# Kernel tuning notes

Measured on AMD Instinct MI355X. Metric: run time of the kernel, lower is better.

The kernel has to match this reference:

```python
import jax, jax.numpy as jnp
import numpy as np

H = 512  # hidden_size

def setup_inputs() -> dict:
    key = jax.random.key(0)
    ks = jax.random.split(key, 5)
    B, S = 2, 512
    feats = jax.random.normal(ks[0], (B, S, H), dtype=jnp.float32)
    # torch Linear init ~ U(-1/sqrt(in), 1/sqrt(in)); scaled normals are fine for a reference
    W1 = jax.random.normal(ks[1], (2 * H, H), dtype=jnp.float32) / np.sqrt(2 * H)
    b1 = jnp.zeros((H,), dtype=jnp.float32)
    W2 = jax.random.normal(ks[2], (H, H // 2), dtype=jnp.float32) / np.sqrt(H)
    b2 = jnp.zeros((H // 2,), dtype=jnp.float32)
    W3 = jax.random.normal(ks[3], (H // 2, 1), dtype=jnp.float32) / np.sqrt(H // 2)
    b3 = jnp.zeros((1,), dtype=jnp.float32)
    return {"features": feats, "W1": W1, "b1": b1, "W2": W2, "b2": b2, "W3": W3, "b3": b3}


def reference(features, W1, b1, W2, b2, W3, b3):
    # cat([f_i, f_j]) @ W1 == f_i @ W1[:H] + f_j @ W1[H:]
    # Precompute the two halves once per residue instead of per pair.
    a = jnp.einsum('bsh,hk->bsk', features, W1[:H])          # [B,S,H]
    c = jnp.einsum('bsh,hk->bsk', features, W1[H:])          # [B,S,H]
    h1 = jax.nn.relu(a[:, :, None, :] + c[:, None, :, :] + b1)  # [B,S,S,H]
    # Dropout(0.1) is identity at inference.
    h2 = jax.nn.relu(jnp.einsum('bijh,hk->bijk', h1, W2) + b2)  # [B,S,S,H//2]
    logits = jnp.einsum('bijk,ko->bijo', h2, W3) + b3            # [B,S,S,1]
    return jax.nn.sigmoid(logits[..., 0])                        # [B,S,S]
```

## Files before the change

kernel.cpp:

```cpp
#include <hip/hip_runtime.h>

#define S_DIM 512
#define H_DIM 512
#define NH 256
#define TI 16
#define TJ 8
#define SROW 520

#define AS1 __attribute__((address_space(1)))
#define AS3 __attribute__((address_space(3)))

typedef _Float16 half8 __attribute__((ext_vector_type(8)));
typedef _Float16 half4 __attribute__((ext_vector_type(4)));
typedef float f32x4 __attribute__((ext_vector_type(4)));
typedef float f32x16 __attribute__((ext_vector_type(16)));

__global__ __launch_bounds__(256) void convert_all_kernel(const float* __restrict__ feats,
        const float* __restrict__ W1, const float* __restrict__ W2,
        _Float16* __restrict__ f16, _Float16* __restrict__ w1L, _Float16* __restrict__ w2L) {
    int blk = blockIdx.x;
    if (blk < 512) {
        int t = blk * 256 + threadIdx.x;
        float4 v = ((const float4*)feats)[t];
        half4 h;
        h.x = (_Float16)v.x; h.y = (_Float16)v.y; h.z = (_Float16)v.z; h.w = (_Float16)v.w;
        ((half4*)f16)[t] = h;
    } else if (blk < 768) {
        int t = (blk - 512) * 256 + threadIdx.x;
        int gcb = t >> 10, n = t & 1023;
        const float* src = (n < H_DIM) ? &W1[(size_t)(gcb * 8) * H_DIM + n]
                                       : &W1[(size_t)(H_DIM + gcb * 8) * H_DIM + (n - H_DIM)];
        half8 v;
#pragma unroll
        for (int j = 0; j < 8; j++) v[j] = (_Float16)src[(size_t)j * H_DIM];
        *(half8*)&w1L[((size_t)gcb * 1024 + n) * 8] = v;
    } else {
        int t = (blk - 768) * 256 + threadIdx.x;
        int gcb = t >> 8, n = t & 255;
        half8 v;
#pragma unroll
        for (int j = 0; j < 8; j++) v[j] = (_Float16)W2[(size_t)(gcb * 8 + j) * NH + n];
        *(half8*)&w2L[((size_t)gcb * 256 + n) * 8] = v;
    }
}

__global__ __launch_bounds__(256) void prep_mfma_kernel(const _Float16* __restrict__ f16,
        const _Float16* __restrict__ w1L, const float* __restrict__ b1,
        _Float16* __restrict__ aH, _Float16* __restrict__ cH) {
    const int tid = threadIdx.x, wave = tid >> 6, lane = tid & 63;
    const int m32 = lane & 31, ch = lane >> 5;
    const int m0 = blockIdx.y * 32;
    const int n0w = blockIdx.x * 128 + wave * 32;
    const int n = n0w + m32;

    const _Float16* ap = &f16[(size_t)(m0 + m32) * H_DIM + ch * 8];
    const _Float16* bp = &w1L[((size_t)ch * 1024 + n) * 8];

    f32x16 acc = (f32x16)0.f;
#pragma unroll
    for (int ks = 0; ks < 32; ks++) {
        half8 af = *(const half8*)&ap[ks * 16];
        half8 bf = *(const half8*)&bp[(size_t)ks * 16384];
        acc = __builtin_amdgcn_mfma_f32_32x32x16_f16(af, bf, acc, 0, 0, 0);
    }
    const bool first_half = (n0w < H_DIM);
    const float bias = first_half ? b1[n & (H_DIM - 1)] : 0.f;
#pragma unroll
    for (int r = 0; r < 16; r++) {
        int m = m0 + (r & 3) + 8 * (r >> 2) + 4 * ch;
        float v = acc[r] + bias;
        if (first_half) aH[(size_t)m * H_DIM + n] = (_Float16)v;
        else            cH[(size_t)m * H_DIM + (n - H_DIM)] = (_Float16)v;
    }
}

__global__ __launch_bounds__(512, 4) void pair_kernel(
        const _Float16* __restrict__ aH, const _Float16* __restrict__ cH,
        const _Float16* __restrict__ w2L,
        const float* __restrict__ b2, const float* __restrict__ W3,
        const float* __restrict__ b3, float* __restrict__ out) {
    const int jt = blockIdx.x, it = blockIdx.y, b = blockIdx.z;
    const int i0 = it * TI, j0 = jt * TJ;

    __shared__ __align__(16) _Float16 sa[TI * SROW];
    __shared__ __align__(16) _Float16 sc[TJ * SROW];
    __shared__ float spart[2 * 64 * 32];

    const int tid = threadIdx.x;
    const int wave = tid >> 6, lane = tid & 63;
    const int mg = wave >> 2, ng = wave & 3;
    const int nb = ng * 64;
    const int m32 = lane & 31, ch = lane >> 5;

#pragma unroll
    for (int rr0 = 0; rr0 < 3; rr0++) {
        int rr = rr0 * 8 + wave;
        if (rr < TI) {
            __builtin_amdgcn_global_load_lds(
                (const AS1 unsigned int*)&aH[((size_t)(b * S_DIM + i0 + rr)) * H_DIM + lane * 8],
                (AS3 unsigned int*)&sa[rr * SROW], 16, 0, 0);
        } else {
            int cr = rr - TI;
            __builtin_amdgcn_global_load_lds(
                (const AS1 unsigned int*)&cH[((size_t)(b * S_DIM + j0 + cr)) * H_DIM + lane * 8],
                (AS3 unsigned int*)&sc[cr * SROW], 16, 0, 0);
        }
    }

    const int il0 = mg * 8 + (m32 >> 3);
    const int il1 = il0 + 4;
    const int jl = m32 & 7;
    const _Float16* vaB0 = &sa[il0 * SROW + ch * 8];
    const _Float16* vaB1 = &sa[il1 * SROW + ch * 8];
    const _Float16* vcB  = &sc[jl * SROW + ch * 8];

    f32x16 acc[2][2];
#pragma unroll
    for (int mt = 0; mt < 2; mt++)
#pragma unroll
        for (int nt = 0; nt < 2; nt++) acc[mt][nt] = (f32x16)0.f;

    const _Float16* bp = &w2L[((size_t)ch * 256 + nb + m32) * 8];
    half8 buf0[2], buf1[2];
    buf0[0] = *(const half8*)&bp[0];
    buf0[1] = *(const half8*)&bp[256];
    buf1[0] = *(const half8*)&bp[4096];
    buf1[1] = *(const half8*)&bp[4096 + 256];

    __syncthreads();

#pragma unroll
    for (int ks = 0; ks < 32; ks++) {
        half8 bf0 = (ks & 1) ? buf1[0] : buf0[0];
        half8 bf1 = (ks & 1) ? buf1[1] : buf0[1];
        if (ks < 30) {
            const _Float16* bn = bp + (size_t)(ks + 2) * 4096;
            if (ks & 1) { buf1[0] = *(const half8*)&bn[0]; buf1[1] = *(const half8*)&bn[256]; }
            else        { buf0[0] = *(const half8*)&bn[0]; buf0[1] = *(const half8*)&bn[256]; }
        }
        half8 vc  = *(const half8*)&vcB[ks * 16];
        half8 va0 = *(const half8*)&vaB0[ks * 16];
        half8 va1 = *(const half8*)&vaB1[ks * 16];
        half8 af0 = __builtin_elementwise_max(va0 + vc, (half8)(_Float16)0.f);
        half8 af1 = __builtin_elementwise_max(va1 + vc, (half8)(_Float16)0.f);
        acc[0][0] = __builtin_amdgcn_mfma_f32_32x32x16_f16(af0, bf0, acc[0][0], 0, 0, 0);
        acc[0][1] = __builtin_amdgcn_mfma_f32_32x32x16_f16(af0, bf1, acc[0][1], 0, 0, 0);
        acc[1][0] = __builtin_amdgcn_mfma_f32_32x32x16_f16(af1, bf0, acc[1][0], 0, 0, 0);
        acc[1][1] = __builtin_amdgcn_mfma_f32_32x32x16_f16(af1, bf1, acc[1][1], 0, 0, 0);
    }

    float b2v[2], w3v[2];
#pragma unroll
    for (int nt = 0; nt < 2; nt++) {
        int n = nb + nt * 32 + m32;
        b2v[nt] = b2[n];
        w3v[nt] = W3[n];
    }
#pragma unroll
    for (int mt = 0; mt < 2; mt++)
#pragma unroll
        for (int r = 0; r < 16; r++) {
            float s = 0.f;
#pragma unroll
            for (int nt = 0; nt < 2; nt++) {
                float v = acc[mt][nt][r] + b2v[nt];
                v = v > 0.f ? v : 0.f;
                s += v * w3v[nt];
            }
            s += __shfl_xor(s, 8);
            s += __shfl_xor(s, 16);
            if (m32 < 8) {
                int row = mt * 32 + (r & 3) + 8 * (r >> 2) + 4 * ch;
                int col = ng * 8 + m32;
                spart[mg * 2048 + row * 32 + ((col + row) & 31)] = s;
            }
        }
    __syncthreads();
    {
        const int R = tid >> 2, sub = tid & 3;
        const int mgf = R >> 6, rowf = R & 63;
        const float* base = &spart[mgf * 2048 + rowf * 32];
        float s = 0.f;
#pragma unroll
        for (int k = 0; k < 8; k++) s += base[(sub * 8 + k + rowf) & 31];
        s += __shfl_xor(s, 1);
        s += __shfl_xor(s, 2);
        if (sub == 0) {
            float tot = s + b3[0];
            float sg = 1.f / (1.f + __expf(-tot));
            int i = i0 + (R >> 3), j = j0 + (R & 7);
            out[(size_t)b * S_DIM * S_DIM + (size_t)i * S_DIM + j] = sg;
        }
    }
}

extern "C" void kernel_launch(void* const* d_in, const int* in_sizes, int n_in,
                              void* d_out, int out_size, void* d_ws, size_t ws_size,
                              hipStream_t stream) {
    const float* feats = (const float*)d_in[0];
    const float* W1 = (const float*)d_in[1];
    const float* b1 = (const float*)d_in[2];
    const float* W2 = (const float*)d_in[3];
    const float* b2 = (const float*)d_in[4];
    const float* W3 = (const float*)d_in[5];
    const float* b3 = (const float*)d_in[6];
    float* out = (float*)d_out;

    const int B = in_sizes[0] / (S_DIM * H_DIM);

    char* ws = (char*)d_ws;
    _Float16* f16  = (_Float16*)ws;
    _Float16* aH   = (_Float16*)(ws + (1 << 20));
    _Float16* cH   = (_Float16*)(ws + (2 << 20));
    _Float16* w1L  = (_Float16*)(ws + (3 << 20));
    _Float16* w2L  = (_Float16*)(ws + (4 << 20));

    convert_all_kernel<<<832, 256, 0, stream>>>(feats, W1, W2, f16, w1L, w2L);
    prep_mfma_kernel<<<dim3(8, 32), 256, 0, stream>>>(f16, w1L, b1, aH, cH);
    pair_kernel<<<dim3(S_DIM / TJ, S_DIM / TI, B), 512, 0, stream>>>(aH, cH, w2L, b2, W3, b3, out);
}
```

Measured before the change: 225.9 us.

## Fuse fp32-to-fp16 conversion into prep GEMM and prefetch LDS operands in pair kernel

Removes the separate conversion pass for features and W1: the prep MFMA kernel now reads fp32 directly and converts in registers, with smaller 128-thread blocks on a wider grid. Only W2 is still pre-converted, by a smaller kernel. In the pair kernel, the LDS reads for the a/c rows are software-pipelined one k-step ahead, and the W2 fragments use an indexed double buffer. This trades an extra launch and global round-trip for strided fp32 column reads of W1 in the prep kernel, plus more registers in the pair kernel.

```diff
diff --git a/kernel.cpp b/kernel.cpp
--- a/kernel.cpp
+++ b/kernel.cpp
@@ -11,66 +11,51 @@
 #define AS3 __attribute__((address_space(3)))
 
 typedef _Float16 half8 __attribute__((ext_vector_type(8)));
-typedef _Float16 half4 __attribute__((ext_vector_type(4)));
-typedef float f32x4 __attribute__((ext_vector_type(4)));
 typedef float f32x16 __attribute__((ext_vector_type(16)));
 
-__global__ __launch_bounds__(256) void convert_all_kernel(const float* __restrict__ feats,
-        const float* __restrict__ W1, const float* __restrict__ W2,
-        _Float16* __restrict__ f16, _Float16* __restrict__ w1L, _Float16* __restrict__ w2L) {
-    int blk = blockIdx.x;
-    if (blk < 512) {
-        int t = blk * 256 + threadIdx.x;
-        float4 v = ((const float4*)feats)[t];
-        half4 h;
-        h.x = (_Float16)v.x; h.y = (_Float16)v.y; h.z = (_Float16)v.z; h.w = (_Float16)v.w;
-        ((half4*)f16)[t] = h;
-    } else if (blk < 768) {
-        int t = (blk - 512) * 256 + threadIdx.x;
-        int gcb = t >> 10, n = t & 1023;
-        const float* src = (n < H_DIM) ? &W1[(size_t)(gcb * 8) * H_DIM + n]
-                                       : &W1[(size_t)(H_DIM + gcb * 8) * H_DIM + (n - H_DIM)];
-        half8 v;
-#pragma unroll
-        for (int j = 0; j < 8; j++) v[j] = (_Float16)src[(size_t)j * H_DIM];
-        *(half8*)&w1L[((size_t)gcb * 1024 + n) * 8] = v;
-    } else {
-        int t = (blk - 768) * 256 + threadIdx.x;
-        int gcb = t >> 8, n = t & 255;
-        half8 v;
-#pragma unroll
-        for (int j = 0; j < 8; j++) v[j] = (_Float16)W2[(size_t)(gcb * 8 + j) * NH + n];
-        *(half8*)&w2L[((size_t)gcb * 256 + n) * 8] = v;
-    }
-}
-
-__global__ __launch_bounds__(256) void prep_mfma_kernel(const _Float16* __restrict__ f16,
-        const _Float16* __restrict__ w1L, const float* __restrict__ b1,
+__global__ __launch_bounds__(256) void convert_w2_kernel(const float* __restrict__ W2,
+                                                         _Float16* __restrict__ w2L) {
+    int t = blockIdx.x * 256 + threadIdx.x;
+    int gcb = t >> 8, n = t & 255;
+    half8 v;
+#pragma unroll
+    for (int j = 0; j < 8; j++) v[j] = (_Float16)W2[(size_t)(gcb * 8 + j) * NH + n];
+    *(half8*)&w2L[((size_t)gcb * 256 + n) * 8] = v;
+}
+
+__global__ __launch_bounds__(128) void prep_mfma_kernel(const float* __restrict__ feats,
+        const float* __restrict__ W1, const float* __restrict__ b1,
         _Float16* __restrict__ aH, _Float16* __restrict__ cH) {
     const int tid = threadIdx.x, wave = tid >> 6, lane = tid & 63;
     const int m32 = lane & 31, ch = lane >> 5;
     const int m0 = blockIdx.y * 32;
-    const int n0w = blockIdx.x * 128 + wave * 32;
-    const int n = n0w + m32;
-
-    const _Float16* ap = &f16[(size_t)(m0 + m32) * H_DIM + ch * 8];
-    const _Float16* bp = &w1L[((size_t)ch * 1024 + n) * 8];
+    const int n = blockIdx.x * 64 + wave * 32 + m32;
+    const bool fh = (n < H_DIM);
+    const float* wcol = fh ? &W1[n] : &W1[(size_t)H_DIM * H_DIM + (n - H_DIM)];
+    const float* arow = &feats[(size_t)(m0 + m32) * H_DIM + ch * 8];
 
     f32x16 acc = (f32x16)0.f;
 #pragma unroll
     for (int ks = 0; ks < 32; ks++) {
-        half8 af = *(const half8*)&ap[ks * 16];
-        half8 bf = *(const half8*)&bp[(size_t)ks * 16384];
+        const int kbase = ks * 16 + ch * 8;
+        float4 a0 = *(const float4*)&arow[ks * 16];
+        float4 a1 = *(const float4*)&arow[ks * 16 + 4];
+        half8 af, bf;
+        af[0] = (_Float16)a0.x; af[1] = (_Float16)a0.y;
+        af[2] = (_Float16)a0.z; af[3] = (_Float16)a0.w;
+        af[4] = (_Float16)a1.x; af[5] = (_Float16)a1.y;
+        af[6] = (_Float16)a1.z; af[7] = (_Float16)a1.w;
+#pragma unroll
+        for (int j = 0; j < 8; j++) bf[j] = (_Float16)wcol[(size_t)(kbase + j) * H_DIM];
         acc = __builtin_amdgcn_mfma_f32_32x32x16_f16(af, bf, acc, 0, 0, 0);
     }
-    const bool first_half = (n0w < H_DIM);
-    const float bias = first_half ? b1[n & (H_DIM - 1)] : 0.f;
+    const float bias = fh ? b1[n] : 0.f;
 #pragma unroll
     for (int r = 0; r < 16; r++) {
         int m = m0 + (r & 3) + 8 * (r >> 2) + 4 * ch;
         float v = acc[r] + bias;
-        if (first_half) aH[(size_t)m * H_DIM + n] = (_Float16)v;
-        else            cH[(size_t)m * H_DIM + (n - H_DIM)] = (_Float16)v;
+        if (fh) aH[(size_t)m * H_DIM + n] = (_Float16)v;
+        else    cH[(size_t)m * H_DIM + (n - H_DIM)] = (_Float16)v;
     }
 }
 
@@ -121,28 +106,35 @@
         for (int nt = 0; nt < 2; nt++) acc[mt][nt] = (f32x16)0.f;
 
     const _Float16* bp = &w2L[((size_t)ch * 256 + nb + m32) * 8];
-    half8 buf0[2], buf1[2];
-    buf0[0] = *(const half8*)&bp[0];
-    buf0[1] = *(const half8*)&bp[256];
-    buf1[0] = *(const half8*)&bp[4096];
-    buf1[1] = *(const half8*)&bp[4096 + 256];
+    half8 bB[2][2];
+    bB[0][0] = *(const half8*)&bp[0];
+    bB[0][1] = *(const half8*)&bp[256];
+    bB[1][0] = *(const half8*)&bp[4096];
+    bB[1][1] = *(const half8*)&bp[4096 + 256];
 
     __syncthreads();
 
+    half8 aB[2][3];
+    aB[0][0] = *(const half8*)&vaB0[0];
+    aB[0][1] = *(const half8*)&vaB1[0];
+    aB[0][2] = *(const half8*)&vcB[0];
+
 #pragma unroll
     for (int ks = 0; ks < 32; ks++) {
-        half8 bf0 = (ks & 1) ? buf1[0] : buf0[0];
-        half8 bf1 = (ks & 1) ? buf1[1] : buf0[1];
+        const int cur = ks & 1, nxt = cur ^ 1;
+        if (ks < 31) {
+            aB[nxt][0] = *(const half8*)&vaB0[(ks + 1) * 16];
+            aB[nxt][1] = *(const half8*)&vaB1[(ks + 1) * 16];
+            aB[nxt][2] = *(const half8*)&vcB[(ks + 1) * 16];
+        }
+        half8 bf0 = bB[cur][0], bf1 = bB[cur][1];
         if (ks < 30) {
             const _Float16* bn = bp + (size_t)(ks + 2) * 4096;
-            if (ks & 1) { buf1[0] = *(const half8*)&bn[0]; buf1[1] = *(const half8*)&bn[256]; }
-            else        { buf0[0] = *(const half8*)&bn[0]; buf0[1] = *(const half8*)&bn[256]; }
-        }
-        half8 vc  = *(const half8*)&vcB[ks * 16];
-        half8 va0 = *(const half8*)&vaB0[ks * 16];
-        half8 va1 = *(const half8*)&vaB1[ks * 16];
-        half8 af0 = __builtin_elementwise_max(va0 + vc, (half8)(_Float16)0.f);
-        half8 af1 = __builtin_elementwise_max(va1 + vc, (half8)(_Float16)0.f);
+            bB[cur][0] = *(const half8*)&bn[0];
+            bB[cur][1] = *(const half8*)&bn[256];
+        }
+        half8 af0 = __builtin_elementwise_max(aB[cur][0] + aB[cur][2], (half8)(_Float16)0.f);
+        half8 af1 = __builtin_elementwise_max(aB[cur][1] + aB[cur][2], (half8)(_Float16)0.f);
         acc[0][0] = __builtin_amdgcn_mfma_f32_32x32x16_f16(af0, bf0, acc[0][0], 0, 0, 0);
         acc[0][1] = __builtin_amdgcn_mfma_f32_32x32x16_f16(af0, bf1, acc[0][1], 0, 0, 0);
         acc[1][0] = __builtin_amdgcn_mfma_f32_32x32x16_f16(af1, bf0, acc[1][0], 0, 0, 0);
@@ -209,13 +201,11 @@
     const int B = in_sizes[0] / (S_DIM * H_DIM);
 
     char* ws = (char*)d_ws;
-    _Float16* f16  = (_Float16*)ws;
-    _Float16* aH   = (_Float16*)(ws + (1 << 20));
-    _Float16* cH   = (_Float16*)(ws + (2 << 20));
-    _Float16* w1L  = (_Float16*)(ws + (3 << 20));
-    _Float16* w2L  = (_Float16*)(ws + (4 << 20));
-
-    convert_all_kernel<<<832, 256, 0, stream>>>(feats, W1, W2, f16, w1L, w2L);
-    prep_mfma_kernel<<<dim3(8, 32), 256, 0, stream>>>(f16, w1L, b1, aH, cH);
+    _Float16* aH   = (_Float16*)ws;
+    _Float16* cH   = (_Float16*)(ws + (1 << 20));
+    _Float16* w2L  = (_Float16*)(ws + (2 << 20));
+
+    convert_w2_kernel<<<64, 256, 0, stream>>>(W2, w2L);
+    prep_mfma_kernel<<<dim3(16, 32), 128, 0, stream>>>(feats, W1, b1, aH, cH);
     pair_kernel<<<dim3(S_DIM / TJ, S_DIM / TI, B), 512, 0, stream>>>(aH, cH, w2L, b2, W3, b3, out);
 }
```

Result: slower. 234.4 us (+3.8%).
